# Performance work log

Measured on AMD Instinct MI355X. Metric: run time of the kernel, lower is better.

## Reference

```python
import jax, jax.numpy as jnp
import numpy as np

ITERATIONS = 3
OUT_CAPS, OUT_DIM = 10, 16


def squash(x):
    # square_norm / (1 + square_norm) * x / (sqrt(square_norm) + 1e-6), norm over last axis
    sn = jnp.sum(x * x, axis=-1, keepdims=True)
    return sn / (1.0 + sn) * x / (jnp.sqrt(sn) + 1e-6)


def setup_inputs() -> dict:
    key = jax.random.key(0)
    kx, kw = jax.random.split(key)
    x = jax.random.normal(kx, (256, 32, 6, 6, 8), dtype=jnp.float32)
    W = 0.01 * jax.random.normal(kw, (1, 32, 6, 6, 10, 8, 16), dtype=jnp.float32)
    return {"x": x, "W": W}


def reference(x, W):
    w = W[0]  # [i,j,k,o,d,e]
    # u_hat: prediction vectors, [B, i, j, k, O, E]
    u_hat = jnp.einsum('bijkd,ijkode->bijkoe', x, w)
    u_det = jax.lax.stop_gradient(u_hat)
    b = jnp.zeros(u_hat.shape[:-1], dtype=u_hat.dtype)  # [B,i,j,k,O]
    for _ in range(ITERATIONS - 1):
        c = jax.nn.softmax(b, axis=-1)
        s = jnp.einsum('bijko,bijkoe->boe', c, u_det)   # reduce over all input-capsule axes
        v = squash(s)                                    # [B,O,E]
        b = b + jnp.einsum('bijkoe,boe->bijko', u_det, v)
    c = jax.nn.softmax(b, axis=-1)
    s = jnp.einsum('bijko,bijkoe->boe', c, u_hat)
    v = squash(s)
    return v.reshape(-1, OUT_CAPS, OUT_DIM)
```

## Files before the change

### kernel.cpp

```cpp
#include <hip/hip_runtime.h>
#include <math.h>

#define BATCH 256
#define IC    1152
#define DD    8
#define OO    10
#define EE    16
#define BTILE 64
#define NBT   4
#define NT    640
#define CHUNK 9
#define NCHUNK 128
#define SJ    3
#define ROUNDS (CHUNK / SJ)

__global__ __launch_bounds__(NT) void caps_pass_kernel(
    const float* __restrict__ x,
    const float* __restrict__ W,
    const float* __restrict__ V,
    float* __restrict__ s_part,
    int first)
{
    __shared__ float x_lds[2][SJ][DD][BTILE];
    __shared__ float logit_lds[2][SJ][NT];

    const int tid = threadIdx.x;
    const int o   = tid >> 6;
    const int bl  = tid & 63;
    const int o_u = __builtin_amdgcn_readfirstlane(o);
    const int b   = blockIdx.y * BTILE + bl;
    const int ijk0 = blockIdx.x * CHUNK;

    float vreg[EE];
    if (first) {
        #pragma unroll
        for (int e = 0; e < EE; ++e) vreg[e] = 0.f;
    } else {
        const float4* vp = reinterpret_cast<const float4*>(V + ((size_t)b * OO + o) * EE);
        #pragma unroll
        for (int q = 0; q < 4; ++q) {
            float4 t = vp[q];
            vreg[q * 4 + 0] = t.x; vreg[q * 4 + 1] = t.y;
            vreg[q * 4 + 2] = t.z; vreg[q * 4 + 3] = t.w;
        }
    }

    float sacc[EE];
    #pragma unroll
    for (int e = 0; e < EE; ++e) sacc[e] = 0.f;

    const bool loader = tid < SJ * BTILE * 2;
    const int ls = tid >> 7;
    const int lr = tid & 127;
    const int lb = lr >> 1;
    const int lq = lr & 1;
    const float* xbase = x + (size_t)(blockIdx.y * BTILE + lb) * (IC * DD) + lq * 4;

    float4 xpre = make_float4(0.f, 0.f, 0.f, 0.f);
    if (loader) xpre = *reinterpret_cast<const float4*>(xbase + (size_t)(ijk0 + ls) * DD);
    if (loader) {
        x_lds[0][ls][lq * 4 + 0][lb] = xpre.x;
        x_lds[0][ls][lq * 4 + 1][lb] = xpre.y;
        x_lds[0][ls][lq * 4 + 2][lb] = xpre.z;
        x_lds[0][ls][lq * 4 + 3][lb] = xpre.w;
    }
    __syncthreads();

    int p = 0;
    for (int r = 0; r < ROUNDS; ++r) {
        if (r + 1 < ROUNDS && loader)
            xpre = *reinterpret_cast<const float4*>(
                xbase + (size_t)(ijk0 + (r + 1) * SJ + ls) * DD);

        float u[SJ][EE];
        float lgr[SJ];
        #pragma unroll
        for (int s = 0; s < SJ; ++s) {
            const int ijk = ijk0 + r * SJ + s;
            const float* wp = W + (size_t)ijk * (OO * DD * EE) + o_u * (DD * EE);
            float xr[DD];
            #pragma unroll
            for (int d = 0; d < DD; ++d) xr[d] = x_lds[p][s][d][bl];
            #pragma unroll
            for (int e = 0; e < EE; ++e) u[s][e] = 0.f;
            #pragma unroll
            for (int d = 0; d < DD; ++d) {
                #pragma unroll
                for (int e = 0; e < EE; ++e)
                    u[s][e] = fmaf(xr[d], wp[d * EE + e], u[s][e]);
            }
            if (!first) {
                float lg = 0.f;
                #pragma unroll
                for (int e = 0; e < EE; ++e) lg += u[s][e] * vreg[e];
                lgr[s] = lg;
                logit_lds[p][s][tid] = lg;
            }
        }

        if (r + 1 < ROUNDS && loader) {
            x_lds[p ^ 1][ls][lq * 4 + 0][lb] = xpre.x;
            x_lds[p ^ 1][ls][lq * 4 + 1][lb] = xpre.y;
            x_lds[p ^ 1][ls][lq * 4 + 2][lb] = xpre.z;
            x_lds[p ^ 1][ls][lq * 4 + 3][lb] = xpre.w;
        }

        __syncthreads();

        if (first) {
            #pragma unroll
            for (int s = 0; s < SJ; ++s)
                #pragma unroll
                for (int e = 0; e < EE; ++e) sacc[e] += 0.1f * u[s][e];
        } else {
            #pragma unroll
            for (int s = 0; s < SJ; ++s) {
                float m = -1e30f;
                #pragma unroll
                for (int oo = 0; oo < OO; ++oo)
                    m = fmaxf(m, logit_lds[p][s][oo * 64 + bl]);
                float den = 0.f;
                #pragma unroll
                for (int oo = 0; oo < OO; ++oo)
                    den += __expf(logit_lds[p][s][oo * 64 + bl] - m);
                float c = __expf(lgr[s] - m) / den;
                #pragma unroll
                for (int e = 0; e < EE; ++e) sacc[e] += c * u[s][e];
            }
        }
        p ^= 1;
    }

    float* sp = s_part + (((size_t)blockIdx.x * BATCH + b) * OO + o) * EE;
    #pragma unroll
    for (int q = 0; q < 4; ++q) {
        float4 t;
        t.x = sacc[q * 4 + 0]; t.y = sacc[q * 4 + 1];
        t.z = sacc[q * 4 + 2]; t.w = sacc[q * 4 + 3];
        reinterpret_cast<float4*>(sp)[q] = t;
    }
}

__global__ __launch_bounds__(256) void caps_squash_kernel(
    const float* __restrict__ s_part,
    float* __restrict__ V,
    float* __restrict__ out,
    int accum, int last)
{
    const int g = blockIdx.x * 256 + threadIdx.x;
    float s = 0.f;
    #pragma unroll 8
    for (int ch = 0; ch < NCHUNK; ++ch)
        s += s_part[(size_t)ch * (BATCH * OO * EE) + g];

    float sq = s * s;
    #pragma unroll
    for (int m = 1; m < 16; m <<= 1) sq += __shfl_xor(sq, m, 16);

    float scale = sq / (1.f + sq) / (sqrtf(sq) + 1e-6f);
    float v = scale * s;

    if (last)       out[g] = v;
    else if (accum) V[g]  += v;
    else            V[g]   = v;
}

extern "C" void kernel_launch(void* const* d_in, const int* in_sizes, int n_in,
                              void* d_out, int out_size, void* d_ws, size_t ws_size,
                              hipStream_t stream) {
    const float* x = (const float*)d_in[0];
    const float* W = (const float*)d_in[1];
    float* out = (float*)d_out;

    float* s_part = (float*)d_ws;
    float* V      = s_part + (size_t)NCHUNK * BATCH * OO * EE;

    dim3 grid(NCHUNK, NBT), blk(NT);
    const int sq_blocks = (BATCH * OO * EE) / 256;

    caps_pass_kernel<<<grid, blk, 0, stream>>>(x, W, V, s_part, 1);
    caps_squash_kernel<<<sq_blocks, 256, 0, stream>>>(s_part, V, out, 0, 0);
    caps_pass_kernel<<<grid, blk, 0, stream>>>(x, W, V, s_part, 0);
    caps_squash_kernel<<<sq_blocks, 256, 0, stream>>>(s_part, V, out, 1, 0);
    caps_pass_kernel<<<grid, blk, 0, stream>>>(x, W, V, s_part, 0);
    caps_squash_kernel<<<sq_blocks, 256, 0, stream>>>(s_part, V, out, 0, 1);
}
```

Baseline: 178.5 us.

## Process two batch rows per thread to reuse W loads across a 128-batch tile

Doubles the batch tile to 128 so each thread computes u for two batch rows and each scalar W load feeds two FMAs. The grid halves in the batch dimension, and the three-capsule round structure is replaced by one input capsule per iteration with a barrier each step. This reduces W traffic per FMA but raises register pressure (two u, v and s arrays) and leaves fewer blocks, which may lower occupancy and add synchronisation.

```diff
diff --git a/kernel.cpp b/kernel.cpp
--- a/kernel.cpp
+++ b/kernel.cpp
@@ -6,13 +6,11 @@
 #define DD    8
 #define OO    10
 #define EE    16
-#define BTILE 64
-#define NBT   4
+#define BTILE 128
+#define NBT   2
 #define NT    640
 #define CHUNK 9
 #define NCHUNK 128
-#define SJ    3
-#define ROUNDS (CHUNK / SJ)
 
 __global__ __launch_bounds__(NT) void caps_pass_kernel(
     const float* __restrict__ x,
@@ -21,123 +19,137 @@
     float* __restrict__ s_part,
     int first)
 {
-    __shared__ float x_lds[2][SJ][DD][BTILE];
-    __shared__ float logit_lds[2][SJ][NT];
+    __shared__ float x_lds[2][DD][BTILE];
+    __shared__ float logit_lds[2][2][OO][64];
 
     const int tid = threadIdx.x;
     const int o   = tid >> 6;
     const int bl  = tid & 63;
     const int o_u = __builtin_amdgcn_readfirstlane(o);
-    const int b   = blockIdx.y * BTILE + bl;
+    const int b0  = blockIdx.y * BTILE + bl;
+    const int b1  = b0 + 64;
     const int ijk0 = blockIdx.x * CHUNK;
 
-    float vreg[EE];
+    float v0[EE], v1[EE];
     if (first) {
         #pragma unroll
-        for (int e = 0; e < EE; ++e) vreg[e] = 0.f;
+        for (int e = 0; e < EE; ++e) { v0[e] = 0.f; v1[e] = 0.f; }
     } else {
-        const float4* vp = reinterpret_cast<const float4*>(V + ((size_t)b * OO + o) * EE);
+        const float4* vp0 = reinterpret_cast<const float4*>(V + ((size_t)b0 * OO + o) * EE);
+        const float4* vp1 = reinterpret_cast<const float4*>(V + ((size_t)b1 * OO + o) * EE);
         #pragma unroll
         for (int q = 0; q < 4; ++q) {
-            float4 t = vp[q];
-            vreg[q * 4 + 0] = t.x; vreg[q * 4 + 1] = t.y;
-            vreg[q * 4 + 2] = t.z; vreg[q * 4 + 3] = t.w;
+            float4 t0 = vp0[q], t1 = vp1[q];
+            v0[q*4+0]=t0.x; v0[q*4+1]=t0.y; v0[q*4+2]=t0.z; v0[q*4+3]=t0.w;
+            v1[q*4+0]=t1.x; v1[q*4+1]=t1.y; v1[q*4+2]=t1.z; v1[q*4+3]=t1.w;
         }
     }
 
-    float sacc[EE];
+    float s0[EE], s1[EE];
     #pragma unroll
-    for (int e = 0; e < EE; ++e) sacc[e] = 0.f;
+    for (int e = 0; e < EE; ++e) { s0[e] = 0.f; s1[e] = 0.f; }
 
-    const bool loader = tid < SJ * BTILE * 2;
-    const int ls = tid >> 7;
-    const int lr = tid & 127;
-    const int lb = lr >> 1;
-    const int lq = lr & 1;
+    const bool loader = tid < BTILE * 2;
+    const int lb = tid >> 1;
+    const int lq = tid & 1;
     const float* xbase = x + (size_t)(blockIdx.y * BTILE + lb) * (IC * DD) + lq * 4;
 
     float4 xpre = make_float4(0.f, 0.f, 0.f, 0.f);
-    if (loader) xpre = *reinterpret_cast<const float4*>(xbase + (size_t)(ijk0 + ls) * DD);
     if (loader) {
-        x_lds[0][ls][lq * 4 + 0][lb] = xpre.x;
-        x_lds[0][ls][lq * 4 + 1][lb] = xpre.y;
-        x_lds[0][ls][lq * 4 + 2][lb] = xpre.z;
-        x_lds[0][ls][lq * 4 + 3][lb] = xpre.w;
+        xpre = *reinterpret_cast<const float4*>(xbase + (size_t)ijk0 * DD);
+        x_lds[0][lq*4+0][lb] = xpre.x;
+        x_lds[0][lq*4+1][lb] = xpre.y;
+        x_lds[0][lq*4+2][lb] = xpre.z;
+        x_lds[0][lq*4+3][lb] = xpre.w;
     }
     __syncthreads();
 
     int p = 0;
-    for (int r = 0; r < ROUNDS; ++r) {
-        if (r + 1 < ROUNDS && loader)
-            xpre = *reinterpret_cast<const float4*>(
-                xbase + (size_t)(ijk0 + (r + 1) * SJ + ls) * DD);
+    for (int r = 0; r < CHUNK; ++r) {
+        const int ijk = ijk0 + r;
 
-        float u[SJ][EE];
-        float lgr[SJ];
+        if (r + 1 < CHUNK && loader)
+            xpre = *reinterpret_cast<const float4*>(xbase + (size_t)(ijk + 1) * DD);
+
+        const float* wp = W + (size_t)ijk * (OO * DD * EE) + o_u * (DD * EE);
+        float u0[EE], u1[EE];
         #pragma unroll
-        for (int s = 0; s < SJ; ++s) {
-            const int ijk = ijk0 + r * SJ + s;
-            const float* wp = W + (size_t)ijk * (OO * DD * EE) + o_u * (DD * EE);
-            float xr[DD];
+        for (int e = 0; e < EE; ++e) { u0[e] = 0.f; u1[e] = 0.f; }
+        #pragma unroll
+        for (int d = 0; d < DD; ++d) {
+            float x0 = x_lds[p][d][bl];
+            float x1 = x_lds[p][d][bl + 64];
             #pragma unroll
-            for (int d = 0; d < DD; ++d) xr[d] = x_lds[p][s][d][bl];
-            #pragma unroll
-            for (int e = 0; e < EE; ++e) u[s][e] = 0.f;
-            #pragma unroll
-            for (int d = 0; d < DD; ++d) {
-                #pragma unroll
-                for (int e = 0; e < EE; ++e)
-                    u[s][e] = fmaf(xr[d], wp[d * EE + e], u[s][e]);
-            }
-            if (!first) {
-                float lg = 0.f;
-                #pragma unroll
-                for (int e = 0; e < EE; ++e) lg += u[s][e] * vreg[e];
-                lgr[s] = lg;
-                logit_lds[p][s][tid] = lg;
+            for (int e = 0; e < EE; ++e) {
+                float w = wp[d * EE + e];
+                u0[e] = fmaf(x0, w, u0[e]);
+                u1[e] = fmaf(x1, w, u1[e]);
             }
         }
 
-        if (r + 1 < ROUNDS && loader) {
-            x_lds[p ^ 1][ls][lq * 4 + 0][lb] = xpre.x;
-            x_lds[p ^ 1][ls][lq * 4 + 1][lb] = xpre.y;
-            x_lds[p ^ 1][ls][lq * 4 + 2][lb] = xpre.z;
-            x_lds[p ^ 1][ls][lq * 4 + 3][lb] = xpre.w;
+        float lg0 = 0.f, lg1 = 0.f;
+        if (!first) {
+            #pragma unroll
+            for (int e = 0; e < EE; ++e) {
+                lg0 = fmaf(u0[e], v0[e], lg0);
+                lg1 = fmaf(u1[e], v1[e], lg1);
+            }
+            logit_lds[p][0][o][bl] = lg0;
+            logit_lds[p][1][o][bl] = lg1;
+        }
+
+        if (r + 1 < CHUNK && loader) {
+            x_lds[p^1][lq*4+0][lb] = xpre.x;
+            x_lds[p^1][lq*4+1][lb] = xpre.y;
+            x_lds[p^1][lq*4+2][lb] = xpre.z;
+            x_lds[p^1][lq*4+3][lb] = xpre.w;
         }
 
         __syncthreads();
 
+        float c0, c1;
         if (first) {
+            c0 = 0.1f; c1 = 0.1f;
+        } else {
+            float l0[OO], l1[OO];
             #pragma unroll
-            for (int s = 0; s < SJ; ++s)
-                #pragma unroll
-                for (int e = 0; e < EE; ++e) sacc[e] += 0.1f * u[s][e];
-        } else {
+            for (int oo = 0; oo < OO; ++oo) {
+                l0[oo] = logit_lds[p][0][oo][bl];
+                l1[oo] = logit_lds[p][1][oo][bl];
+            }
+            float m0 = -1e30f, m1 = -1e30f;
             #pragma unroll
-            for (int s = 0; s < SJ; ++s) {
-                float m = -1e30f;
-                #pragma unroll
-                for (int oo = 0; oo < OO; ++oo)
-                    m = fmaxf(m, logit_lds[p][s][oo * 64 + bl]);
-                float den = 0.f;
-                #pragma unroll
-                for (int oo = 0; oo < OO; ++oo)
-                    den += __expf(logit_lds[p][s][oo * 64 + bl] - m);
-                float c = __expf(lgr[s] - m) / den;
-                #pragma unroll
-                for (int e = 0; e < EE; ++e) sacc[e] += c * u[s][e];
+            for (int oo = 0; oo < OO; ++oo) {
+                m0 = fmaxf(m0, l0[oo]);
+                m1 = fmaxf(m1, l1[oo]);
             }
+            float d0 = 0.f, d1 = 0.f;
+            #pragma unroll
+            for (int oo = 0; oo < OO; ++oo) {
+                d0 += __expf(l0[oo] - m0);
+                d1 += __expf(l1[oo] - m1);
+            }
+            c0 = __expf(lg0 - m0) / d0;
+            c1 = __expf(lg1 - m1) / d1;
+        }
+
+        #pragma unroll
+        for (int e = 0; e < EE; ++e) {
+            s0[e] = fmaf(c0, u0[e], s0[e]);
+            s1[e] = fmaf(c1, u1[e], s1[e]);
         }
         p ^= 1;
     }
 
-    float* sp = s_part + (((size_t)blockIdx.x * BATCH + b) * OO + o) * EE;
+    float* sp0 = s_part + (((size_t)blockIdx.x * BATCH + b0) * OO + o) * EE;
+    float* sp1 = s_part + (((size_t)blockIdx.x * BATCH + b1) * OO + o) * EE;
     #pragma unroll
     for (int q = 0; q < 4; ++q) {
-        float4 t;
-        t.x = sacc[q * 4 + 0]; t.y = sacc[q * 4 + 1];
-        t.z = sacc[q * 4 + 2]; t.w = sacc[q * 4 + 3];
-        reinterpret_cast<float4*>(sp)[q] = t;
+        float4 t0, t1;
+        t0.x = s0[q*4+0]; t0.y = s0[q*4+1]; t0.z = s0[q*4+2]; t0.w = s0[q*4+3];
+        t1.x = s1[q*4+0]; t1.y = s1[q*4+1]; t1.z = s1[q*4+2]; t1.w = s1[q*4+3];
+        reinterpret_cast<float4*>(sp0)[q] = t0;
+        reinterpret_cast<float4*>(sp1)[q] = t1;
     }
 }
 
```

Result: faster. 173.6 us (-2.8%).
